# Kernel optimization log

Measured on AMD Instinct MI355X. Metric: run time of the kernel, lower is better.

Reference implementation:

```python
import jax, jax.numpy as jnp
import numpy as np

B, N, C = 8, 512, 64
VOCAB = 200000
TEMP = 0.07
THR = 0.99
EPS = 1e-8


def _norm(x):
    # torch F.normalize: x / clamp(||x||, min=eps)
    return x / jnp.maximum(jnp.linalg.norm(x, axis=-1, keepdims=True), EPS)


def setup_inputs() -> dict:
    key = jax.random.key(0)
    k = jax.random.split(key, 6)
    return {
        "Q": jax.random.normal(k[0], (B, N, C), dtype=jnp.float32),
        "Pos": jax.random.normal(k[1], (B, N, C), dtype=jnp.float32),
        "neg_global": jax.random.normal(k[2], (B, N, C), dtype=jnp.float32),
        "pos_item_ids": jax.random.randint(k[3], (B, N), 0, VOCAB),
        "neg_global_item_ids": jax.random.randint(k[4], (B, N), 0, VOCAB),
        "log_q_table": jax.random.normal(k[5], (VOCAB,), dtype=jnp.float32),
    }


def reference(Q, Pos, neg_global, pos_item_ids, neg_global_item_ids, log_q_table):
    B_, N_, C_ = Q.shape
    BN = B_ * N_
    Qn, Pn, Gn = _norm(Q), _norm(Pos), _norm(neg_global)
    Qf = Qn.reshape(BN, C_)
    Pf = Pn.reshape(BN, C_)
    Nf = Gn.reshape(BN, C_)
    pos_ids = pos_item_ids.reshape(BN)
    neg_ids = neg_global_item_ids.reshape(BN)
    row_seq = jnp.arange(BN) // N_  # sequence index of each flattened row
    neg_inf = jnp.float32(-jnp.inf)

    # ---- global negatives ----
    p2n = (Pf @ Nf.T).reshape(B_, N_, BN)            # (B, N, BN) cosine Pos vs neg
    ok_glob = (jnp.max(p2n, axis=1) <= THR)[row_seq]  # (BN, BN) per-seq max mask
    sim_glob = (Qf @ Nf.T) / TEMP
    logits_glob = jnp.where(ok_glob, sim_glob - log_q_table[neg_ids][None, :], neg_inf)

    # ---- in-batch negatives ----
    p2p = (Pf @ Pf.T).reshape(B_, N_, BN)
    diff_seq = row_seq[:, None] != row_seq[None, :]
    ok_ibn = (jnp.max(p2p, axis=1) <= THR)[row_seq] & diff_seq
    sim_ibn = (Qf @ Pf.T) / TEMP
    logits_ibn = jnp.where(ok_ibn, sim_ibn - log_q_table[pos_ids][None, :], neg_inf)

    # ---- positive logits ----
    pos_logits = (jnp.sum(Qn * Pn, axis=-1) / TEMP).reshape(BN, 1)
    pos_logits = pos_logits - log_q_table[pos_ids][:, None]

    # concat: (BN, 1 + 2*BN)
    return jnp.concatenate([pos_logits, logits_glob, logits_ibn], axis=1)
```

## Files before the change

### kernel.cpp

```cpp
#include <hip/hip_runtime.h>
#include <math.h>

#define B_  8
#define N_  512
#define C_  64
#define BN  4096
#define OUTW 8193
#define INV_TEMP 14.285714285714286f
#define THR_ 0.99f
#define NEG_HUGE -1e30f

typedef __attribute__((ext_vector_type(8))) short short8v;
typedef __attribute__((ext_vector_type(4))) float f32x4;

#define WSB_QN   0
#define WSB_PN   (512*1024)
#define WSB_GN   (1024*1024)
#define WSB_LQP  (1536*1024)
#define WSB_LQN  (WSB_LQP + 16*1024)
#define WSB_MAXG (WSB_LQP + 32*1024)
#define WSB_MAXI (WSB_MAXG + 128*1024)

__device__ __forceinline__ unsigned short f2bf(float f) {
  unsigned u = __float_as_uint(f);
  u += 0x7fffu + ((u >> 16) & 1u);
  return (unsigned short)(u >> 16);
}

__global__ __launch_bounds__(256) void knorm(const float* __restrict__ Q,
    const float* __restrict__ P, const float* __restrict__ G,
    unsigned short* __restrict__ wbf) {
  int gw   = blockIdx.x * 4 + (threadIdx.x >> 6);
  int lane = threadIdx.x & 63;
  int t = gw >> 12, r = gw & 4095;
  const float* src = (t == 0) ? Q : (t == 1 ? P : G);
  unsigned short* dst = wbf + (size_t)t * BN * C_;
  float x = src[(size_t)r * C_ + lane];
  float s = x * x;
  #pragma unroll
  for (int off = 32; off; off >>= 1) s += __shfl_xor(s, off);
  float inv = 1.0f / fmaxf(sqrtf(s), 1e-8f);
  dst[(size_t)r * C_ + lane] = f2bf(x * inv);
}

__global__ __launch_bounds__(256) void kpos(const float* __restrict__ Q,
    const float* __restrict__ P,
    const int* __restrict__ pos_ids, const int* __restrict__ neg_ids,
    const float* __restrict__ table, float* __restrict__ lqp,
    float* __restrict__ lqn, float* __restrict__ out) {
  int i    = blockIdx.x * 4 + (threadIdx.x >> 6);
  int lane = threadIdx.x & 63;
  float q = Q[(size_t)i * C_ + lane];
  float p = P[(size_t)i * C_ + lane];
  float qq = q * q, pp = p * p, qp = q * p;
  #pragma unroll
  for (int off = 32; off; off >>= 1) {
    qq += __shfl_xor(qq, off);
    pp += __shfl_xor(pp, off);
    qp += __shfl_xor(qp, off);
  }
  if (lane == 0) {
    float d = qp / (fmaxf(sqrtf(qq), 1e-8f) * fmaxf(sqrtf(pp), 1e-8f));
    float lp = table[pos_ids[i]];
    out[(size_t)i * OUTW] = d * INV_TEMP - lp;
    lqp[i] = lp;
    lqn[i] = table[neg_ids[i]];
  }
}

__global__ __launch_bounds__(256) void kmaskM(const unsigned short* __restrict__ PN,
    const unsigned short* __restrict__ GN, float* __restrict__ maxout) {
  __shared__ uint4 A4[1024];
  __shared__ uint4 B4[1024];
  __shared__ float red[2][128];
  int tid = threadIdx.x;
  int jt = blockIdx.x, b = blockIdx.y, z = blockIdx.z;
  const unsigned short* X = z ? PN : GN;
  int j0 = jt * 128;

  #pragma unroll
  for (int it = 0; it < 4; ++it) {
    int idx = tid + 256 * it, row = idx >> 3, kc = idx & 7;
    B4[row * 8 + (kc ^ (row & 7))] =
        *(const uint4*)(X + (size_t)(j0 + row) * C_ + kc * 8);
  }
  int wid = tid >> 6, lane = tid & 63;
  int m0 = (wid >> 1) * 64, n0 = (wid & 1) * 64;
  int lr = lane & 15, lk = lane >> 4;
  const short8v* As = (const short8v*)A4;
  const short8v* Bs = (const short8v*)B4;
  float mcol[4] = {NEG_HUGE, NEG_HUGE, NEG_HUGE, NEG_HUGE};

  for (int ch = 0; ch < 4; ++ch) {
    __syncthreads();
    #pragma unroll
    for (int it = 0; it < 4; ++it) {
      int idx = tid + 256 * it, row = idx >> 3, kc = idx & 7;
      A4[row * 8 + (kc ^ (row & 7))] =
          *(const uint4*)(PN + (size_t)(b * N_ + ch * 128 + row) * C_ + kc * 8);
    }
    __syncthreads();

    f32x4 zz = {0.f, 0.f, 0.f, 0.f};
    f32x4 acc[4][4];
    #pragma unroll
    for (int mf = 0; mf < 4; ++mf)
      #pragma unroll
      for (int nf = 0; nf < 4; ++nf) acc[mf][nf] = zz;

    #pragma unroll
    for (int ks = 0; ks < 2; ++ks) {
      int kc = lk + ks * 4;
      short8v a[4], bgs[4];
      #pragma unroll
      for (int mf = 0; mf < 4; ++mf) {
        int r = m0 + mf * 16 + lr;
        a[mf] = As[r * 8 + (kc ^ (r & 7))];
      }
      #pragma unroll
      for (int nf = 0; nf < 4; ++nf) {
        int r = n0 + nf * 16 + lr;
        bgs[nf] = Bs[r * 8 + (kc ^ (r & 7))];
      }
      #pragma unroll
      for (int mf = 0; mf < 4; ++mf)
        #pragma unroll
        for (int nf = 0; nf < 4; ++nf)
          acc[mf][nf] = __builtin_amdgcn_mfma_f32_16x16x32_bf16(
              a[mf], bgs[nf], acc[mf][nf], 0, 0, 0);
    }
    #pragma unroll
    for (int nf = 0; nf < 4; ++nf)
      #pragma unroll
      for (int mf = 0; mf < 4; ++mf)
        #pragma unroll
        for (int rg = 0; rg < 4; ++rg)
          mcol[nf] = fmaxf(mcol[nf], acc[mf][nf][rg]);
  }
  #pragma unroll
  for (int nf = 0; nf < 4; ++nf) {
    float v = mcol[nf];
    v = fmaxf(v, __shfl_xor(v, 16));
    v = fmaxf(v, __shfl_xor(v, 32));
    mcol[nf] = v;
  }
  int wn = wid >> 1, wj = wid & 1;
  if (lane < 16) {
    #pragma unroll
    for (int nf = 0; nf < 4; ++nf)
      red[wn][wj * 64 + nf * 16 + lane] = mcol[nf];
  }
  __syncthreads();
  if (tid < 128)
    maxout[(size_t)(z * 8 + b) * 4096 + j0 + tid] =
        fmaxf(red[0][tid], red[1][tid]);
}

__global__ __launch_bounds__(256) void klogitsM(const unsigned short* __restrict__ QN,
    const unsigned short* __restrict__ PN, const unsigned short* __restrict__ GN,
    const float* __restrict__ lqp, const float* __restrict__ lqn,
    const float* __restrict__ maxg, const float* __restrict__ maxi,
    float* __restrict__ out) {
  __shared__ uint4 A4[1024];
  __shared__ uint4 B4[1024];
  __shared__ float oks[128];
  __shared__ float lqs[128];
  int tid = threadIdx.x;
  int jt = blockIdx.x, half = jt >> 5;
  int j0 = (jt & 31) * 128;
  int i0 = blockIdx.y * 128;
  size_t colbase = 1 + (size_t)half * BN + j0;

  if (half && ((i0 >> 9) == (j0 >> 9))) {
    #pragma unroll
    for (int it = 0; it < 16; ++it) {
      int idx = tid + 256 * it;
      int row = idx >> 5, c4 = (idx & 31) * 4;
      float* p = out + (size_t)(i0 + row) * OUTW + colbase + c4;
      p[0] = NEG_HUGE; p[1] = NEG_HUGE; p[2] = NEG_HUGE; p[3] = NEG_HUGE;
    }
    return;
  }

  const unsigned short* X = half ? PN : GN;
  const float* lq = half ? lqp : lqn;
  const float* mc = (half ? maxi : maxg) + (size_t)(i0 >> 9) * 4096;

  if (tid < 128) {
    oks[tid] = (mc[j0 + tid] <= THR_) ? 1.0f : 0.0f;
    lqs[tid] = lq[j0 + tid];
  }
  #pragma unroll
  for (int it = 0; it < 4; ++it) {
    int idx = tid + 256 * it, row = idx >> 3, kc = idx & 7;
    A4[row * 8 + (kc ^ (row & 7))] =
        *(const uint4*)(QN + (size_t)(i0 + row) * C_ + kc * 8);
    B4[row * 8 + (kc ^ (row & 7))] =
        *(const uint4*)(X + (size_t)(j0 + row) * C_ + kc * 8);
  }
  __syncthreads();

  int wid = tid >> 6, lane = tid & 63;
  int m0 = (wid >> 1) * 64, n0 = (wid & 1) * 64;
  int lr = lane & 15, lk = lane >> 4;
  const short8v* As = (const short8v*)A4;
  const short8v* Bs = (const short8v*)B4;

  f32x4 zz = {0.f, 0.f, 0.f, 0.f};
  f32x4 acc[4][4];
  #pragma unroll
  for (int mf = 0; mf < 4; ++mf)
    #pragma unroll
    for (int nf = 0; nf < 4; ++nf) acc[mf][nf] = zz;

  #pragma unroll
  for (int ks = 0; ks < 2; ++ks) {
    int kc = lk + ks * 4;
    short8v a[4], bgs[4];
    #pragma unroll
    for (int mf = 0; mf < 4; ++mf) {
      int r = m0 + mf * 16 + lr;
      a[mf] = As[r * 8 + (kc ^ (r & 7))];
    }
    #pragma unroll
    for (int nf = 0; nf < 4; ++nf) {
      int r = n0 + nf * 16 + lr;
      bgs[nf] = Bs[r * 8 + (kc ^ (r & 7))];
    }
    #pragma unroll
    for (int mf = 0; mf < 4; ++mf)
      #pragma unroll
      for (int nf = 0; nf < 4; ++nf)
        acc[mf][nf] = __builtin_amdgcn_mfma_f32_16x16x32_bf16(
            a[mf], bgs[nf], acc[mf][nf], 0, 0, 0);
  }

  int rbase = i0 + m0 + lk * 4;
  #pragma unroll
  for (int nf = 0; nf < 4; ++nf) {
    int j = n0 + nf * 16 + lr;
    float okv = oks[j];
    float lqv = lqs[j];
    #pragma unroll
    for (int mf = 0; mf < 4; ++mf) {
      size_t base = (size_t)(rbase + mf * 16) * OUTW + colbase + j;
      #pragma unroll
      for (int rg = 0; rg < 4; ++rg) {
        float v = acc[mf][nf][rg] * INV_TEMP - lqv;
        out[base + (size_t)rg * OUTW] = (okv != 0.0f) ? v : NEG_HUGE;
      }
    }
  }
}

extern "C" void kernel_launch(void* const* d_in, const int* in_sizes, int n_in,
                              void* d_out, int out_size, void* d_ws, size_t ws_size,
                              hipStream_t stream) {
  const float* Q = (const float*)d_in[0];
  const float* P = (const float*)d_in[1];
  const float* G = (const float*)d_in[2];
  const int* pos_ids = (const int*)d_in[3];
  const int* neg_ids = (const int*)d_in[4];
  const float* table = (const float*)d_in[5];
  float* out = (float*)d_out;
  char* w = (char*)d_ws;
  unsigned short* QN = (unsigned short*)(w + WSB_QN);
  unsigned short* PN = (unsigned short*)(w + WSB_PN);
  unsigned short* GN = (unsigned short*)(w + WSB_GN);
  float* LQP = (float*)(w + WSB_LQP);
  float* LQN = (float*)(w + WSB_LQN);
  float* MAXG = (float*)(w + WSB_MAXG);
  float* MAXI = (float*)(w + WSB_MAXI);

  knorm<<<dim3(3 * BN / 4), 256, 0, stream>>>(Q, P, G, QN);
  kpos<<<dim3(BN / 4), 256, 0, stream>>>(Q, P, pos_ids, neg_ids, table,
                                         LQP, LQN, out);
  kmaskM<<<dim3(32, 8, 2), 256, 0, stream>>>(PN, GN, MAXG);
  klogitsM<<<dim3(64, 32), 256, 0, stream>>>(QN, PN, GN, LQP, LQN,
                                             MAXG, MAXI, out);
}
```

Baseline: 184.0 us.

## Fuse prep kernels, use direct global-to-LDS loads, vectorize masked stores

Merges the normalization and positive-logit kernels into one launch, reusing the already-loaded Q row and its norm. Tile loads in the mask and logits GEMM kernels now go straight from global memory to LDS through the global_load_lds builtin, with the swizzle moved to the source address. The all-masked in-batch block stores float4 values instead of scalar stores. The aim is fewer launches, fewer register round-trips, and fewer store instructions, at the cost of relying on the semantics of the direct-to-LDS path.

```diff
diff --git a/kernel.cpp b/kernel.cpp
--- a/kernel.cpp
+++ b/kernel.cpp
@@ -27,44 +27,43 @@
   return (unsigned short)(u >> 16);
 }
 
-__global__ __launch_bounds__(256) void knorm(const float* __restrict__ Q,
+__device__ __forceinline__ void load_lds16(const void* g, void* l) {
+  __builtin_amdgcn_global_load_lds(
+      (const __attribute__((address_space(1))) unsigned int*)g,
+      (__attribute__((address_space(3))) unsigned int*)l, 16, 0, 0);
+}
+
+__global__ __launch_bounds__(256) void kprep(const float* __restrict__ Q,
     const float* __restrict__ P, const float* __restrict__ G,
-    unsigned short* __restrict__ wbf) {
+    const int* __restrict__ pos_ids, const int* __restrict__ neg_ids,
+    const float* __restrict__ table, unsigned short* __restrict__ wbf,
+    float* __restrict__ lqp, float* __restrict__ lqn, float* __restrict__ out) {
   int gw   = blockIdx.x * 4 + (threadIdx.x >> 6);
   int lane = threadIdx.x & 63;
   int t = gw >> 12, r = gw & 4095;
   const float* src = (t == 0) ? Q : (t == 1 ? P : G);
-  unsigned short* dst = wbf + (size_t)t * BN * C_;
   float x = src[(size_t)r * C_ + lane];
   float s = x * x;
   #pragma unroll
   for (int off = 32; off; off >>= 1) s += __shfl_xor(s, off);
   float inv = 1.0f / fmaxf(sqrtf(s), 1e-8f);
-  dst[(size_t)r * C_ + lane] = f2bf(x * inv);
-}
-
-__global__ __launch_bounds__(256) void kpos(const float* __restrict__ Q,
-    const float* __restrict__ P,
-    const int* __restrict__ pos_ids, const int* __restrict__ neg_ids,
-    const float* __restrict__ table, float* __restrict__ lqp,
-    float* __restrict__ lqn, float* __restrict__ out) {
-  int i    = blockIdx.x * 4 + (threadIdx.x >> 6);
-  int lane = threadIdx.x & 63;
-  float q = Q[(size_t)i * C_ + lane];
-  float p = P[(size_t)i * C_ + lane];
-  float qq = q * q, pp = p * p, qp = q * p;
-  #pragma unroll
-  for (int off = 32; off; off >>= 1) {
-    qq += __shfl_xor(qq, off);
-    pp += __shfl_xor(pp, off);
-    qp += __shfl_xor(qp, off);
-  }
-  if (lane == 0) {
-    float d = qp / (fmaxf(sqrtf(qq), 1e-8f) * fmaxf(sqrtf(pp), 1e-8f));
-    float lp = table[pos_ids[i]];
-    out[(size_t)i * OUTW] = d * INV_TEMP - lp;
-    lqp[i] = lp;
-    lqn[i] = table[neg_ids[i]];
+  wbf[(size_t)t * BN * C_ + (size_t)r * C_ + lane] = f2bf(x * inv);
+
+  if (t == 0) {
+    float p = P[(size_t)r * C_ + lane];
+    float pp = p * p, qp = x * p;
+    #pragma unroll
+    for (int off = 32; off; off >>= 1) {
+      pp += __shfl_xor(pp, off);
+      qp += __shfl_xor(qp, off);
+    }
+    if (lane == 0) {
+      float d = qp / (fmaxf(sqrtf(s), 1e-8f) * fmaxf(sqrtf(pp), 1e-8f));
+      float lp = table[pos_ids[r]];
+      out[(size_t)r * OUTW] = d * INV_TEMP - lp;
+      lqp[r] = lp;
+      lqn[r] = table[neg_ids[r]];
+    }
   }
 }
 
@@ -81,8 +80,7 @@
   #pragma unroll
   for (int it = 0; it < 4; ++it) {
     int idx = tid + 256 * it, row = idx >> 3, kc = idx & 7;
-    B4[row * 8 + (kc ^ (row & 7))] =
-        *(const uint4*)(X + (size_t)(j0 + row) * C_ + kc * 8);
+    load_lds16(X + (size_t)(j0 + row) * C_ + (kc ^ (row & 7)) * 8, &B4[idx]);
   }
   int wid = tid >> 6, lane = tid & 63;
   int m0 = (wid >> 1) * 64, n0 = (wid & 1) * 64;
@@ -96,8 +94,8 @@
     #pragma unroll
     for (int it = 0; it < 4; ++it) {
       int idx = tid + 256 * it, row = idx >> 3, kc = idx & 7;
-      A4[row * 8 + (kc ^ (row & 7))] =
-          *(const uint4*)(PN + (size_t)(b * N_ + ch * 128 + row) * C_ + kc * 8);
+      load_lds16(PN + (size_t)(b * N_ + ch * 128 + row) * C_ + (kc ^ (row & 7)) * 8,
+                 &A4[idx]);
     }
     __syncthreads();
 
@@ -172,12 +170,12 @@
   size_t colbase = 1 + (size_t)half * BN + j0;
 
   if (half && ((i0 >> 9) == (j0 >> 9))) {
+    float4 nh = {NEG_HUGE, NEG_HUGE, NEG_HUGE, NEG_HUGE};
     #pragma unroll
     for (int it = 0; it < 16; ++it) {
       int idx = tid + 256 * it;
       int row = idx >> 5, c4 = (idx & 31) * 4;
-      float* p = out + (size_t)(i0 + row) * OUTW + colbase + c4;
-      p[0] = NEG_HUGE; p[1] = NEG_HUGE; p[2] = NEG_HUGE; p[3] = NEG_HUGE;
+      *(float4*)(out + (size_t)(i0 + row) * OUTW + colbase + c4) = nh;
     }
     return;
   }
@@ -193,10 +191,9 @@
   #pragma unroll
   for (int it = 0; it < 4; ++it) {
     int idx = tid + 256 * it, row = idx >> 3, kc = idx & 7;
-    A4[row * 8 + (kc ^ (row & 7))] =
-        *(const uint4*)(QN + (size_t)(i0 + row) * C_ + kc * 8);
-    B4[row * 8 + (kc ^ (row & 7))] =
-        *(const uint4*)(X + (size_t)(j0 + row) * C_ + kc * 8);
+    int sc = (kc ^ (row & 7)) * 8;
+    load_lds16(QN + (size_t)(i0 + row) * C_ + sc, &A4[idx]);
+    load_lds16(X  + (size_t)(j0 + row) * C_ + sc, &B4[idx]);
   }
   __syncthreads();
 
@@ -272,9 +269,8 @@
   float* MAXG = (float*)(w + WSB_MAXG);
   float* MAXI = (float*)(w + WSB_MAXI);
 
-  knorm<<<dim3(3 * BN / 4), 256, 0, stream>>>(Q, P, G, QN);
-  kpos<<<dim3(BN / 4), 256, 0, stream>>>(Q, P, pos_ids, neg_ids, table,
-                                         LQP, LQN, out);
+  kprep<<<dim3(3 * BN / 4), 256, 0, stream>>>(Q, P, G, pos_ids, neg_ids, table,
+                                              QN, LQP, LQN, out);
   kmaskM<<<dim3(32, 8, 2), 256, 0, stream>>>(PN, GN, MAXG);
   klogitsM<<<dim3(64, 32), 256, 0, stream>>>(QN, PN, GN, LQP, LQN,
                                              MAXG, MAXI, out);
```

After: 182.1 us. No clear change (-1.0%).
